# Kernel tuning notes

Hardware: AMD Instinct MI355X
Metric: run time of the kernel (lower is better)

Reference implementation:

```python
import jax, jax.numpy as jnp
import numpy as np

N, T, HID, H = 2, 2048, 1024, 16
D = HID // H


def setup_inputs() -> dict:
    key = jax.random.key(0)
    ks = jax.random.split(key, 11)
    s = 1.0 / np.sqrt(HID)
    return {
        "q": jax.random.normal(ks[0], (N, T, HID), jnp.float32),
        "k": jax.random.normal(ks[1], (N, T, HID), jnp.float32),
        "v": jax.random.normal(ks[2], (N, T, HID), jnp.float32),
        "Wq": jax.random.normal(ks[3], (HID, HID), jnp.float32) * s,
        "bq": jnp.zeros((HID,), jnp.float32),
        "Wk": jax.random.normal(ks[4], (HID, HID), jnp.float32) * s,
        "bk": jnp.zeros((HID,), jnp.float32),
        "Wv": jax.random.normal(ks[5], (HID, HID), jnp.float32) * s,
        "bv": jnp.zeros((HID,), jnp.float32),
        "Wo": jax.random.normal(ks[6], (HID, HID), jnp.float32) * s,
        "bo": jnp.zeros((HID,), jnp.float32),
    }


def reference(q, k, v, Wq, bq, Wk, bk, Wv, bv, Wo, bo):
    n, t, _ = q.shape
    # Linear projections, then the original's quirky head split:
    # .view(N, H, T, D) directly from (N, T, H*D) (no transpose).
    qh = (q @ Wq + bq).reshape(n, H, t, D)
    kh = (k @ Wk + bk).reshape(n, H, t, D)
    vh = (v @ Wv + bv).reshape(n, H, t, D)
    # scores: (N, H, T, T), scaled by sqrt(hidden_size) (not head dim)
    scores = jnp.einsum("nhtd,nhsd->nhts", qh, kh) / jnp.sqrt(jnp.float32(HID))
    # faithful quirk: softmax over dim=1 (the head axis)
    attn = jax.nn.softmax(scores, axis=1)
    # dropout is identity (eval / drop_rate=0)
    out = jnp.einsum("nhts,nhsd->nhtd", attn, vh).reshape(n, t, H * D)
    return out @ Wo + bo
```

## Files before the change

kernel.cpp:

```cpp
#include <hip/hip_runtime.h>

typedef unsigned short u16;
typedef __bf16 bf16x8 __attribute__((ext_vector_type(8)));
typedef float f32x4 __attribute__((ext_vector_type(4)));

#define MFMA16 __builtin_amdgcn_mfma_f32_16x16x32_bf16

constexpr int NB = 2, TS = 2048, HD = 1024, NH = 16, DH = 64;
constexpr float ALPHA = 0.045084220027780106f;

__device__ __forceinline__ u16 f2bf(float f) {
    union { float f; unsigned u; } v; v.f = f;
    unsigned r = v.u + 0x7FFFu + ((v.u >> 16) & 1u);
    return (u16)(r >> 16);
}
__device__ __forceinline__ float bf2f(u16 h) {
    union { unsigned u; float f; } v; v.u = ((unsigned)h) << 16;
    return v.f;
}
__device__ __forceinline__ bf16x8 ldb8(const u16* p) {
    return *reinterpret_cast<const bf16x8*>(p);
}
__device__ __forceinline__ void glds16(const u16* g, u16* l) {
    __builtin_amdgcn_global_load_lds(
        (const __attribute__((address_space(1))) unsigned int*)g,
        (__attribute__((address_space(3))) unsigned int*)l, 16, 0, 0);
}

#if defined(__has_builtin)
#  if __has_builtin(__builtin_amdgcn_cvt_pk_bf16_f32)
#    define HAVE_PKBF16 1
#  endif
#  if __has_builtin(__builtin_amdgcn_exp2f)
#    define HAVE_EXP2 1
#  endif
#endif
#ifndef HAVE_PKBF16
#  define HAVE_PKBF16 0
#endif
#ifndef HAVE_EXP2
#  define HAVE_EXP2 0
#endif
__device__ __forceinline__ unsigned pk2(float a, float b) {
#if HAVE_PKBF16
    typedef __bf16 bf16x2 __attribute__((ext_vector_type(2)));
    bf16x2 r = __builtin_amdgcn_cvt_pk_bf16_f32(a, b);
    return __builtin_bit_cast(unsigned, r);
#else
    return (unsigned)f2bf(a) | ((unsigned)f2bf(b) << 16);
#endif
}
__device__ __forceinline__ float fexp2(float x) {
#if HAVE_EXP2
    return __builtin_amdgcn_exp2f(x);
#else
    return exp2f(x);
#endif
}

__global__ __launch_bounds__(256) void to_bf16(
    const float* __restrict__ a0, const float* __restrict__ a1, const float* __restrict__ a2,
    u16* __restrict__ o0, u16* __restrict__ o1, u16* __restrict__ o2)
{
    const float* s; u16* d;
    if (blockIdx.y == 0)      { s = a0; d = o0; }
    else if (blockIdx.y == 1) { s = a1; d = o1; }
    else                      { s = a2; d = o2; }
    size_t i = ((size_t)blockIdx.x * 256 + threadIdx.x) * 8;
    float4 v0 = *reinterpret_cast<const float4*>(s + i);
    float4 v1 = *reinterpret_cast<const float4*>(s + i + 4);
    uint4 w = { pk2(v0.x, v0.y), pk2(v0.z, v0.w), pk2(v1.x, v1.y), pk2(v1.z, v1.w) };
    *reinterpret_cast<uint4*>(d + i) = w;
}

__global__ __launch_bounds__(256) void wtrans(
    const float* __restrict__ w0, const float* __restrict__ w1,
    const float* __restrict__ w2, const float* __restrict__ w3,
    u16* __restrict__ o0, u16* __restrict__ o1,
    u16* __restrict__ o2, u16* __restrict__ o3)
{
    const float* src; u16* dst; float sc;
    if (blockIdx.z == 0)      { src = w0; dst = o0; sc = ALPHA; }
    else if (blockIdx.z == 1) { src = w1; dst = o1; sc = 1.0f; }
    else if (blockIdx.z == 2) { src = w2; dst = o2; sc = 1.0f; }
    else                      { src = w3; dst = o3; sc = 1.0f; }
    __shared__ __align__(16) u16 tile[64 * 72];
    const int k0 = blockIdx.y * 64, n0 = blockIdx.x * 64;
    const int t = threadIdx.x, r = t >> 2, c0 = (t & 3) << 4;
#pragma unroll
    for (int j = 0; j < 4; ++j) {
        float4 v = *reinterpret_cast<const float4*>(&src[(size_t)(k0 + r) * HD + n0 + c0 + 4 * j]);
        tile[(c0 + 4 * j + 0) * 72 + r] = f2bf(v.x * sc);
        tile[(c0 + 4 * j + 1) * 72 + r] = f2bf(v.y * sc);
        tile[(c0 + 4 * j + 2) * 72 + r] = f2bf(v.z * sc);
        tile[(c0 + 4 * j + 3) * 72 + r] = f2bf(v.w * sc);
    }
    __syncthreads();
#pragma unroll
    for (int j = 0; j < 2; ++j)
        *reinterpret_cast<uint4*>(&dst[(size_t)(n0 + r) * HD + k0 + c0 + 8 * j]) =
            *reinterpret_cast<const uint4*>(&tile[r * 72 + c0 + 8 * j]);
}

__global__ __launch_bounds__(256) void gemm_qkv(
    const u16* __restrict__ A0, const u16* __restrict__ A1, const u16* __restrict__ A2,
    const u16* __restrict__ B0, const u16* __restrict__ B1, const u16* __restrict__ B2,
    const float* __restrict__ c0, const float* __restrict__ c1, const float* __restrict__ c2,
    u16* __restrict__ C0, u16* __restrict__ C1, u16* __restrict__ C2)
{
    const u16 *A, *BT; const float* bias; u16* C; float bsc;
    if (blockIdx.z == 0)      { A = A0; BT = B0; bias = c0; C = C0; bsc = ALPHA; }
    else if (blockIdx.z == 1) { A = A1; BT = B1; bias = c1; C = C1; bsc = 1.0f; }
    else                      { A = A2; BT = B2; bias = c2; C = C2; bsc = 1.0f; }
    constexpr int N = HD, K = HD;
    __shared__ __align__(16) u16 As[128 * 32];
    __shared__ __align__(16) u16 Bs[128 * 32];
    const int m0 = blockIdx.y * 128, n0 = blockIdx.x * 128;
    const int tid = threadIdx.x, wid = tid >> 6, lane = tid & 63;
    const int q = lane >> 4, c = lane & 15;
    const int wm = wid >> 1, wn = wid & 1;
    const int srow = tid >> 2, scol = (tid & 3) << 3;
    const u16* ag0 = A + (size_t)(m0 + srow) * K + scol;
    const u16* ag1 = A + (size_t)(m0 + 64 + srow) * K + scol;
    const u16* bg0 = BT + (size_t)(n0 + srow) * K + scol;
    const u16* bg1 = BT + (size_t)(n0 + 64 + srow) * K + scol;
    f32x4 acc[4][4] = {};
    for (int k0 = 0; k0 < K; k0 += 32) {
        glds16(ag0, &As[tid * 8]);
        glds16(ag1, &As[2048 + tid * 8]);
        glds16(bg0, &Bs[tid * 8]);
        glds16(bg1, &Bs[2048 + tid * 8]);
        ag0 += 32; ag1 += 32; bg0 += 32; bg1 += 32;
        __syncthreads();
        bf16x8 af[4], bf[4];
#pragma unroll
        for (int i = 0; i < 4; ++i)  af[i] = ldb8(&As[(wm * 64 + i * 16 + c) * 32 + q * 8]);
#pragma unroll
        for (int jn = 0; jn < 4; ++jn) bf[jn] = ldb8(&Bs[(wn * 64 + jn * 16 + c) * 32 + q * 8]);
#pragma unroll
        for (int i = 0; i < 4; ++i)
#pragma unroll
            for (int jn = 0; jn < 4; ++jn)
                acc[i][jn] = MFMA16(bf[jn], af[i], acc[i][jn], 0, 0, 0);
        __syncthreads();
    }
#pragma unroll
    for (int i = 0; i < 4; ++i)
#pragma unroll
        for (int jn = 0; jn < 4; ++jn) {
            int row = m0 + wm * 64 + i * 16 + c;
            int col = n0 + wn * 64 + jn * 16 + q * 4;
            float4 bb = *reinterpret_cast<const float4*>(&bias[col]);
            uint2 w = { pk2(acc[i][jn][0] + bb.x * bsc, acc[i][jn][1] + bb.y * bsc),
                        pk2(acc[i][jn][2] + bb.z * bsc, acc[i][jn][3] + bb.w * bsc) };
            *reinterpret_cast<uint2*>(&C[(size_t)row * N + col]) = w;
        }
}

__global__ __launch_bounds__(256) void vtrans(const u16* __restrict__ V, u16* __restrict__ VT)
{
    __shared__ __align__(16) u16 tile[64 * 72];
    const int nh = blockIdx.y, t0 = blockIdx.x * 64;
    const u16* src = V + (size_t)nh * TS * DH;
    u16* dst = VT + (size_t)nh * DH * TS;
    const int t = threadIdx.x, r = t >> 2, c0 = (t & 3) << 4;
    *reinterpret_cast<uint4*>(&tile[r * 72 + c0]) =
        *reinterpret_cast<const uint4*>(&src[(size_t)(t0 + r) * DH + c0]);
    *reinterpret_cast<uint4*>(&tile[r * 72 + c0 + 8]) =
        *reinterpret_cast<const uint4*>(&src[(size_t)(t0 + r) * DH + c0 + 8]);
    __syncthreads();
    const int d = t >> 2, tc = (t & 3) << 4;
    u16 tmp[16];
#pragma unroll
    for (int j = 0; j < 16; ++j) tmp[j] = tile[(tc + j) * 72 + d];
    *reinterpret_cast<uint4*>(&dst[(size_t)d * TS + t0 + tc]) = *reinterpret_cast<const uint4*>(&tmp[0]);
    *reinterpret_cast<uint4*>(&dst[(size_t)d * TS + t0 + tc + 8]) = *reinterpret_cast<const uint4*>(&tmp[8]);
}

__global__ __launch_bounds__(256) void gemm_out(
    const u16* __restrict__ A, const u16* __restrict__ BT,
    const float* __restrict__ bias, float* __restrict__ C,
    int M, int N, int K)
{
    __shared__ __align__(16) u16 As[64 * 32];
    __shared__ __align__(16) u16 Bs[128 * 32];
    const int m0 = blockIdx.y * 64, n0 = blockIdx.x * 128;
    const int tid = threadIdx.x, wid = tid >> 6, lane = tid & 63;
    const int q = lane >> 4, c = lane & 15;
    const int wm = wid >> 1, wn = wid & 1;
    const int arow = tid >> 2, acol = (tid & 3) << 3;
    const u16* ag = A + (size_t)(m0 + arow) * K + acol;
    const u16* bg0 = BT + (size_t)(n0 + arow) * K + acol;
    const u16* bg1 = BT + (size_t)(n0 + 64 + arow) * K + acol;
    f32x4 acc[2][4] = {};
    for (int k0 = 0; k0 < K; k0 += 32) {
        glds16(ag, &As[tid * 8]);
        glds16(bg0, &Bs[tid * 8]);
        glds16(bg1, &Bs[2048 + tid * 8]);
        ag += 32; bg0 += 32; bg1 += 32;
        __syncthreads();
        bf16x8 af[2], bf[4];
#pragma unroll
        for (int jm = 0; jm < 2; ++jm) af[jm] = ldb8(&As[(wm * 32 + jm * 16 + c) * 32 + q * 8]);
#pragma unroll
        for (int jn = 0; jn < 4; ++jn) bf[jn] = ldb8(&Bs[(wn * 64 + jn * 16 + c) * 32 + q * 8]);
#pragma unroll
        for (int jm = 0; jm < 2; ++jm)
#pragma unroll
            for (int jn = 0; jn < 4; ++jn)
                acc[jm][jn] = MFMA16(bf[jn], af[jm], acc[jm][jn], 0, 0, 0);
        __syncthreads();
    }
#pragma unroll
    for (int jm = 0; jm < 2; ++jm)
#pragma unroll
        for (int jn = 0; jn < 4; ++jn) {
            int row = m0 + wm * 32 + jm * 16 + c;
            int col = n0 + wn * 64 + jn * 16 + q * 4;
            float4 bb = *reinterpret_cast<const float4*>(&bias[col]);
            float4 v = { acc[jm][jn][0] + bb.x, acc[jm][jn][1] + bb.y,
                         acc[jm][jn][2] + bb.z, acc[jm][jn][3] + bb.w };
            *reinterpret_cast<float4*>(&C[(size_t)row * N + col]) = v;
        }
}

__global__ __launch_bounds__(256) void z_kernel(
    const u16* __restrict__ Qp, const u16* __restrict__ Kp, u16* __restrict__ Zf)
{
    __shared__ __align__(16) u16 Ks[64 * 64];
    __shared__ __align__(16) u16 Qs[128 * 64];
    const int sb = blockIdx.x, tb = blockIdx.y, n = blockIdx.z;
    const int s0 = sb * 64, t0 = tb * 128;
    const int tid = threadIdx.x, wid = tid >> 6, lane = tid & 63;
    const int q = lane >> 4, c = lane & 15;
    const int krow = tid >> 3, kch = tid & 7;
    const int xsw = (kch ^ (krow & 7)) << 3;
    const u16* kg0 = Kp + (size_t)(n * NH) * TS * DH + (size_t)(s0 + krow) * DH + xsw;
    const u16* qg0 = Qp + (size_t)(n * NH) * TS * DH + (size_t)(t0 + krow) * DH + xsw;
    float zacc[2][4][4] = {};
    for (int h = 0; h < NH; ++h) {
        glds16(kg0, &Ks[tid * 8]);
        glds16(kg0 + (size_t)32 * DH, &Ks[2048 + tid * 8]);
#pragma unroll
        for (int L = 0; L < 4; ++L)
            glds16(qg0 + (size_t)(L * 32) * DH, &Qs[L * 2048 + tid * 8]);
        kg0 += (size_t)TS * DH; qg0 += (size_t)TS * DH;
        __syncthreads();
        bf16x8 qa[2][2], kb[4][2];
#pragma unroll
        for (int jm = 0; jm < 2; ++jm)
#pragma unroll
            for (int kf = 0; kf < 2; ++kf)
                qa[jm][kf] = ldb8(&Qs[(wid * 32 + jm * 16 + c) * 64 + (((kf * 4 + q) ^ (c & 7)) << 3)]);
#pragma unroll
        for (int i = 0; i < 4; ++i)
#pragma unroll
            for (int kf = 0; kf < 2; ++kf)
                kb[i][kf] = ldb8(&Ks[(i * 16 + c) * 64 + (((kf * 4 + q) ^ (c & 7)) << 3)]);
        f32x4 s_[2][4] = {};
#pragma unroll
        for (int kf = 0; kf < 2; ++kf)
#pragma unroll
            for (int jm = 0; jm < 2; ++jm)
#pragma unroll
                for (int i = 0; i < 4; ++i)
                    s_[jm][i] = MFMA16(kb[i][kf], qa[jm][kf], s_[jm][i], 0, 0, 0);
#pragma unroll
        for (int jm = 0; jm < 2; ++jm)
#pragma unroll
            for (int i = 0; i < 4; ++i)
#pragma unroll
                for (int r = 0; r < 4; ++r)
                    zacc[jm][i][r] += fexp2(s_[jm][i][r]);
        __syncthreads();
    }
#pragma unroll
    for (int jm = 0; jm < 2; ++jm) {
        int t = t0 + wid * 32 + jm * 16 + c;
        size_t zb = ((size_t)((n * 32 + sb) * 2048) + t) * 64 + q * 16;
        unsigned w32[8];
#pragma unroll
        for (int i = 0; i < 4; ++i) {
            w32[i * 2 + 0] = pk2(1.0f / zacc[jm][i][0], 1.0f / zacc[jm][i][1]);
            w32[i * 2 + 1] = pk2(1.0f / zacc[jm][i][2], 1.0f / zacc[jm][i][3]);
        }
        *reinterpret_cast<uint4*>(&Zf[zb])     = *reinterpret_cast<const uint4*>(&w32[0]);
        *reinterpret_cast<uint4*>(&Zf[zb + 8]) = *reinterpret_cast<const uint4*>(&w32[4]);
    }
}

__global__ __launch_bounds__(256) void attn_kernel(
    const u16* __restrict__ Qp, const u16* __restrict__ Kp, const u16* __restrict__ VT,
    const u16* __restrict__ Zf, u16* __restrict__ o2)
{
    __shared__ __align__(16) u16 Ks[64 * 64];
    __shared__ __align__(16) u16 Vs[64 * 64];
    __shared__ __align__(16) u16 Ps[64 * 72];
    const int tb = blockIdx.x, h = blockIdx.y, n = blockIdx.z;
    const int t0 = tb * 64;
    const int tid = threadIdx.x, wid = tid >> 6, lane = tid & 63;
    const int q = lane >> 4, c = lane & 15;
    const int krow = tid >> 3, kch = tid & 7;
    const int xsw = (kch ^ (krow & 7)) << 3;
    const size_t base = (size_t)(n * NH + h) * TS * DH;
    const u16* Qh = Qp + base;
    const int tme = t0 + wid * 16 + c;
    bf16x8 qa[2];
#pragma unroll
    for (int kf = 0; kf < 2; ++kf)
        qa[kf] = ldb8(&Qh[(size_t)tme * DH + kf * 32 + q * 8]);
    const u16* kg0 = Kp + base + (size_t)krow * DH + xsw;
    const u16* kg1 = kg0 + (size_t)32 * DH;
    const u16* vg0 = VT + base + (size_t)krow * TS + xsw;
    const u16* vg1 = vg0 + (size_t)32 * TS;
    const u16* zg  = Zf + ((size_t)(n * 32) * 2048 + tme) * 64 + q * 16;
    f32x4 oacc[4] = {};
    for (int sb = 0; sb < 32; ++sb) {
        glds16(kg0, &Ks[tid * 8]);
        glds16(kg1, &Ks[2048 + tid * 8]);
        glds16(vg0, &Vs[tid * 8]);
        glds16(vg1, &Vs[2048 + tid * 8]);
        u16 zl[16];
        *reinterpret_cast<uint4*>(&zl[0]) = *reinterpret_cast<const uint4*>(zg);
        *reinterpret_cast<uint4*>(&zl[8]) = *reinterpret_cast<const uint4*>(zg + 8);
        kg0 += 64 * DH; kg1 += 64 * DH; vg0 += 64; vg1 += 64; zg += (size_t)2048 * 64;
        __syncthreads();
        bf16x8 kb[4][2];
#pragma unroll
        for (int i = 0; i < 4; ++i)
#pragma unroll
            for (int kf = 0; kf < 2; ++kf)
                kb[i][kf] = ldb8(&Ks[(i * 16 + c) * 64 + (((kf * 4 + q) ^ (c & 7)) << 3)]);
        f32x4 s_[4] = {};
#pragma unroll
        for (int kf = 0; kf < 2; ++kf)
#pragma unroll
            for (int i = 0; i < 4; ++i)
                s_[i] = MFMA16(kb[i][kf], qa[kf], s_[i], 0, 0, 0);
#pragma unroll
        for (int i = 0; i < 4; ++i) {
            float p0 = fexp2(s_[i][0]) * bf2f(zl[i * 4 + 0]);
            float p1 = fexp2(s_[i][1]) * bf2f(zl[i * 4 + 1]);
            float p2 = fexp2(s_[i][2]) * bf2f(zl[i * 4 + 2]);
            float p3 = fexp2(s_[i][3]) * bf2f(zl[i * 4 + 3]);
            uint2 w = { pk2(p0, p1), pk2(p2, p3) };
            *reinterpret_cast<uint2*>(&Ps[(wid * 16 + c) * 72 + i * 16 + q * 4]) = w;
        }
        bf16x8 pa[2], vb[4][2];
#pragma unroll
        for (int kf = 0; kf < 2; ++kf)
            pa[kf] = ldb8(&Ps[(wid * 16 + c) * 72 + kf * 32 + q * 8]);
#pragma unroll
        for (int dn = 0; dn < 4; ++dn)
#pragma unroll
            for (int kf = 0; kf < 2; ++kf)
                vb[dn][kf] = ldb8(&Vs[(dn * 16 + c) * 64 + (((kf * 4 + q) ^ (c & 7)) << 3)]);
#pragma unroll
        for (int kf = 0; kf < 2; ++kf)
#pragma unroll
            for (int dn = 0; dn < 4; ++dn)
                oacc[dn] = MFMA16(vb[dn][kf], pa[kf], oacc[dn], 0, 0, 0);
        __syncthreads();
    }
#pragma unroll
    for (int dn = 0; dn < 4; ++dn) {
        uint2 w = { pk2(oacc[dn][0], oacc[dn][1]), pk2(oacc[dn][2], oacc[dn][3]) };
        *reinterpret_cast<uint2*>(&o2[base + (size_t)tme * DH + dn * 16 + q * 4]) = w;
    }
}

extern "C" void kernel_launch(void* const* d_in, const int* in_sizes, int n_in,
                              void* d_out, int out_size, void* d_ws, size_t ws_size,
                              hipStream_t stream)
{
    const float* q  = (const float*)d_in[0];
    const float* k  = (const float*)d_in[1];
    const float* v  = (const float*)d_in[2];
    const float* Wq = (const float*)d_in[3];
    const float* bq = (const float*)d_in[4];
    const float* Wk = (const float*)d_in[5];
    const float* bk = (const float*)d_in[6];
    const float* Wv = (const float*)d_in[7];
    const float* bv = (const float*)d_in[8];
    const float* Wo = (const float*)d_in[9];
    const float* bo = (const float*)d_in[10];
    float* out = (float*)d_out;

    u16* ws  = (u16*)d_ws;
    u16* wqT = ws + 0 * 1048576;
    u16* wkT = ws + 1 * 1048576;
    u16* wvT = ws + 2 * 1048576;
    u16* woT = ws + 3 * 1048576;
    u16* S1  = ws + 4194304;
    u16* S2  = S1 + 4194304;
    u16* S3  = S2 + 4194304;
    u16* S4  = S3 + 4194304;
    u16* S5  = S4 + 4194304;
    u16* S6  = S5 + 4194304;
    u16 *qb = S1, *kb = S2, *vb = S3;
    u16 *Qp = S4, *Kp = S5, *Vp = S6;
    u16 *VTb = S1, *Zf = S2, *o2 = S6;

    to_bf16<<<dim3(2048, 3), 256, 0, stream>>>(q, k, v, qb, kb, vb);
    wtrans<<<dim3(16, 16, 4), 256, 0, stream>>>(Wq, Wk, Wv, Wo, wqT, wkT, wvT, woT);
    gemm_qkv<<<dim3(8, 32, 3), 256, 0, stream>>>(qb, kb, vb, wqT, wkT, wvT,
                                                 bq, bk, bv, Qp, Kp, Vp);
    vtrans<<<dim3(32, 32), 256, 0, stream>>>(Vp, VTb);
    z_kernel<<<dim3(32, 16, 2), 256, 0, stream>>>(Qp, Kp, Zf);
    attn_kernel<<<dim3(32, 16, 2), 256, 0, stream>>>(Qp, Kp, VTb, Zf, o2);
    gemm_out<<<dim3(8, 64), 256, 0, stream>>>(o2, woT, bo, out, NB * TS, HD, HD);
}
```

Measured before the change: 295.4 us.

## Merge prep kernels, widen GEMM K-tiles, double-buffer attention and Z loads

Merges the input bf16 conversion and weight transpose into one launch. Both GEMMs now use a 64-wide K step with XOR-swizzled shared memory, which halves the number of barriers per tile. The attention and Z kernels double-buffer their K/V shared tiles so the next block loads while the current one computes. The Z kernel also reads Q fragments straight from global memory instead of staging them in LDS. The cost is more LDS use per block, which may lower occupancy, and Q reads in the Z kernel are no longer coalesced through shared memory.

New measurement: 325.4 us. 10.2% more time.

```diff
diff --git a/kernel.cpp b/kernel.cpp
--- a/kernel.cpp
+++ b/kernel.cpp
@@ -58,34 +58,36 @@
 #endif
 }
 
-__global__ __launch_bounds__(256) void to_bf16(
+__global__ __launch_bounds__(256) void prep(
     const float* __restrict__ a0, const float* __restrict__ a1, const float* __restrict__ a2,
-    u16* __restrict__ o0, u16* __restrict__ o1, u16* __restrict__ o2)
-{
-    const float* s; u16* d;
-    if (blockIdx.y == 0)      { s = a0; d = o0; }
-    else if (blockIdx.y == 1) { s = a1; d = o1; }
-    else                      { s = a2; d = o2; }
-    size_t i = ((size_t)blockIdx.x * 256 + threadIdx.x) * 8;
-    float4 v0 = *reinterpret_cast<const float4*>(s + i);
-    float4 v1 = *reinterpret_cast<const float4*>(s + i + 4);
-    uint4 w = { pk2(v0.x, v0.y), pk2(v0.z, v0.w), pk2(v1.x, v1.y), pk2(v1.z, v1.w) };
-    *reinterpret_cast<uint4*>(d + i) = w;
-}
-
-__global__ __launch_bounds__(256) void wtrans(
+    u16* __restrict__ o0, u16* __restrict__ o1, u16* __restrict__ o2,
     const float* __restrict__ w0, const float* __restrict__ w1,
     const float* __restrict__ w2, const float* __restrict__ w3,
-    u16* __restrict__ o0, u16* __restrict__ o1,
-    u16* __restrict__ o2, u16* __restrict__ o3)
-{
-    const float* src; u16* dst; float sc;
-    if (blockIdx.z == 0)      { src = w0; dst = o0; sc = ALPHA; }
-    else if (blockIdx.z == 1) { src = w1; dst = o1; sc = 1.0f; }
-    else if (blockIdx.z == 2) { src = w2; dst = o2; sc = 1.0f; }
-    else                      { src = w3; dst = o3; sc = 1.0f; }
+    u16* __restrict__ wo0, u16* __restrict__ wo1,
+    u16* __restrict__ wo2, u16* __restrict__ wo3)
+{
     __shared__ __align__(16) u16 tile[64 * 72];
-    const int k0 = blockIdx.y * 64, n0 = blockIdx.x * 64;
+    if (blockIdx.z < 3) {
+        const float* s; u16* d;
+        if (blockIdx.z == 0)      { s = a0; d = o0; }
+        else if (blockIdx.z == 1) { s = a1; d = o1; }
+        else                      { s = a2; d = o2; }
+        size_t i = ((size_t)blockIdx.x * 256 + threadIdx.x) * 8;
+        float4 v0 = *reinterpret_cast<const float4*>(s + i);
+        float4 v1 = *reinterpret_cast<const float4*>(s + i + 4);
+        uint4 w = { pk2(v0.x, v0.y), pk2(v0.z, v0.w), pk2(v1.x, v1.y), pk2(v1.z, v1.w) };
+        *reinterpret_cast<uint4*>(d + i) = w;
+        return;
+    }
+    if (blockIdx.x >= 1024) return;
+    const int wi = blockIdx.x >> 8, ti = blockIdx.x & 255;
+    const int ky = ti >> 4, nx = ti & 15;
+    const float* src; u16* dst; float sc = 1.0f;
+    if (wi == 0)      { src = w0; dst = wo0; sc = ALPHA; }
+    else if (wi == 1) { src = w1; dst = wo1; }
+    else if (wi == 2) { src = w2; dst = wo2; }
+    else              { src = w3; dst = wo3; }
+    const int k0 = ky * 64, n0 = nx * 64;
     const int t = threadIdx.x, r = t >> 2, c0 = (t & 3) << 4;
 #pragma unroll
     for (int j = 0; j < 4; ++j) {
@@ -113,35 +115,40 @@
     else if (blockIdx.z == 1) { A = A1; BT = B1; bias = c1; C = C1; bsc = 1.0f; }
     else                      { A = A2; BT = B2; bias = c2; C = C2; bsc = 1.0f; }
     constexpr int N = HD, K = HD;
-    __shared__ __align__(16) u16 As[128 * 32];
-    __shared__ __align__(16) u16 Bs[128 * 32];
+    __shared__ __align__(16) u16 As[128 * 64];
+    __shared__ __align__(16) u16 Bs[128 * 64];
     const int m0 = blockIdx.y * 128, n0 = blockIdx.x * 128;
     const int tid = threadIdx.x, wid = tid >> 6, lane = tid & 63;
     const int q = lane >> 4, c = lane & 15;
     const int wm = wid >> 1, wn = wid & 1;
-    const int srow = tid >> 2, scol = (tid & 3) << 3;
-    const u16* ag0 = A + (size_t)(m0 + srow) * K + scol;
-    const u16* ag1 = A + (size_t)(m0 + 64 + srow) * K + scol;
-    const u16* bg0 = BT + (size_t)(n0 + srow) * K + scol;
-    const u16* bg1 = BT + (size_t)(n0 + 64 + srow) * K + scol;
+    const int r = tid >> 3, ch = tid & 7;
+    const int xc = (ch ^ (r & 7)) << 3;
+    const u16* ag = A + (size_t)(m0 + r) * K + xc;
+    const u16* bg = BT + (size_t)(n0 + r) * K + xc;
     f32x4 acc[4][4] = {};
-    for (int k0 = 0; k0 < K; k0 += 32) {
-        glds16(ag0, &As[tid * 8]);
-        glds16(ag1, &As[2048 + tid * 8]);
-        glds16(bg0, &Bs[tid * 8]);
-        glds16(bg1, &Bs[2048 + tid * 8]);
-        ag0 += 32; ag1 += 32; bg0 += 32; bg1 += 32;
-        __syncthreads();
-        bf16x8 af[4], bf[4];
-#pragma unroll
-        for (int i = 0; i < 4; ++i)  af[i] = ldb8(&As[(wm * 64 + i * 16 + c) * 32 + q * 8]);
-#pragma unroll
-        for (int jn = 0; jn < 4; ++jn) bf[jn] = ldb8(&Bs[(wn * 64 + jn * 16 + c) * 32 + q * 8]);
+    for (int k0 = 0; k0 < K; k0 += 64) {
+#pragma unroll
+        for (int L = 0; L < 4; ++L) {
+            glds16(ag + (size_t)(32 * L) * K, &As[L * 2048 + tid * 8]);
+            glds16(bg + (size_t)(32 * L) * K, &Bs[L * 2048 + tid * 8]);
+        }
+        ag += 64; bg += 64;
+        __syncthreads();
+        bf16x8 af[4][2], bf[4][2];
 #pragma unroll
         for (int i = 0; i < 4; ++i)
 #pragma unroll
-            for (int jn = 0; jn < 4; ++jn)
-                acc[i][jn] = MFMA16(bf[jn], af[i], acc[i][jn], 0, 0, 0);
+            for (int kk = 0; kk < 2; ++kk) {
+                af[i][kk] = ldb8(&As[(wm * 64 + i * 16 + c) * 64 + (((kk * 4 + q) ^ (c & 7)) << 3)]);
+                bf[i][kk] = ldb8(&Bs[(wn * 64 + i * 16 + c) * 64 + (((kk * 4 + q) ^ (c & 7)) << 3)]);
+            }
+#pragma unroll
+        for (int kk = 0; kk < 2; ++kk)
+#pragma unroll
+            for (int i = 0; i < 4; ++i)
+#pragma unroll
+                for (int jn = 0; jn < 4; ++jn)
+                    acc[i][jn] = MFMA16(bf[jn][kk], af[i][kk], acc[i][jn], 0, 0, 0);
         __syncthreads();
     }
 #pragma unroll
@@ -182,33 +189,43 @@
     const float* __restrict__ bias, float* __restrict__ C,
     int M, int N, int K)
 {
-    __shared__ __align__(16) u16 As[64 * 32];
-    __shared__ __align__(16) u16 Bs[128 * 32];
+    __shared__ __align__(16) u16 As[64 * 64];
+    __shared__ __align__(16) u16 Bs[128 * 64];
     const int m0 = blockIdx.y * 64, n0 = blockIdx.x * 128;
     const int tid = threadIdx.x, wid = tid >> 6, lane = tid & 63;
     const int q = lane >> 4, c = lane & 15;
     const int wm = wid >> 1, wn = wid & 1;
-    const int arow = tid >> 2, acol = (tid & 3) << 3;
-    const u16* ag = A + (size_t)(m0 + arow) * K + acol;
-    const u16* bg0 = BT + (size_t)(n0 + arow) * K + acol;
-    const u16* bg1 = BT + (size_t)(n0 + 64 + arow) * K + acol;
+    const int r = tid >> 3, ch = tid & 7;
+    const int xc = (ch ^ (r & 7)) << 3;
+    const u16* ag = A + (size_t)(m0 + r) * K + xc;
+    const u16* bg = BT + (size_t)(n0 + r) * K + xc;
     f32x4 acc[2][4] = {};
-    for (int k0 = 0; k0 < K; k0 += 32) {
+    for (int k0 = 0; k0 < K; k0 += 64) {
         glds16(ag, &As[tid * 8]);
-        glds16(bg0, &Bs[tid * 8]);
-        glds16(bg1, &Bs[2048 + tid * 8]);
-        ag += 32; bg0 += 32; bg1 += 32;
-        __syncthreads();
-        bf16x8 af[2], bf[4];
-#pragma unroll
-        for (int jm = 0; jm < 2; ++jm) af[jm] = ldb8(&As[(wm * 32 + jm * 16 + c) * 32 + q * 8]);
-#pragma unroll
-        for (int jn = 0; jn < 4; ++jn) bf[jn] = ldb8(&Bs[(wn * 64 + jn * 16 + c) * 32 + q * 8]);
+        glds16(ag + (size_t)32 * K, &As[2048 + tid * 8]);
+#pragma unroll
+        for (int L = 0; L < 4; ++L)
+            glds16(bg + (size_t)(32 * L) * K, &Bs[L * 2048 + tid * 8]);
+        ag += 64; bg += 64;
+        __syncthreads();
+        bf16x8 af[2][2], bf[4][2];
 #pragma unroll
         for (int jm = 0; jm < 2; ++jm)
 #pragma unroll
-            for (int jn = 0; jn < 4; ++jn)
-                acc[jm][jn] = MFMA16(bf[jn], af[jm], acc[jm][jn], 0, 0, 0);
+            for (int kk = 0; kk < 2; ++kk)
+                af[jm][kk] = ldb8(&As[(wm * 32 + jm * 16 + c) * 64 + (((kk * 4 + q) ^ (c & 7)) << 3)]);
+#pragma unroll
+        for (int jn = 0; jn < 4; ++jn)
+#pragma unroll
+            for (int kk = 0; kk < 2; ++kk)
+                bf[jn][kk] = ldb8(&Bs[(wn * 64 + jn * 16 + c) * 64 + (((kk * 4 + q) ^ (c & 7)) << 3)]);
+#pragma unroll
+        for (int kk = 0; kk < 2; ++kk)
+#pragma unroll
+            for (int jm = 0; jm < 2; ++jm)
+#pragma unroll
+                for (int jn = 0; jn < 4; ++jn)
+                    acc[jm][jn] = MFMA16(bf[jn][kk], af[jm][kk], acc[jm][jn], 0, 0, 0);
         __syncthreads();
     }
 #pragma unroll
@@ -227,36 +244,39 @@
 __global__ __launch_bounds__(256) void z_kernel(
     const u16* __restrict__ Qp, const u16* __restrict__ Kp, u16* __restrict__ Zf)
 {
-    __shared__ __align__(16) u16 Ks[64 * 64];
-    __shared__ __align__(16) u16 Qs[128 * 64];
+    __shared__ __align__(16) u16 Ks[2 * 64 * 64];
     const int sb = blockIdx.x, tb = blockIdx.y, n = blockIdx.z;
     const int s0 = sb * 64, t0 = tb * 128;
     const int tid = threadIdx.x, wid = tid >> 6, lane = tid & 63;
     const int q = lane >> 4, c = lane & 15;
     const int krow = tid >> 3, kch = tid & 7;
     const int xsw = (kch ^ (krow & 7)) << 3;
-    const u16* kg0 = Kp + (size_t)(n * NH) * TS * DH + (size_t)(s0 + krow) * DH + xsw;
-    const u16* qg0 = Qp + (size_t)(n * NH) * TS * DH + (size_t)(t0 + krow) * DH + xsw;
+    const u16* kg = Kp + (size_t)(n * NH) * TS * DH + (size_t)(s0 + krow) * DH + xsw;
+    const u16* Qh = Qp + (size_t)(n * NH) * TS * DH;
+    glds16(kg, &Ks[tid * 8]);
+    glds16(kg + (size_t)32 * DH, &Ks[2048 + tid * 8]);
+    kg += (size_t)TS * DH;
     float zacc[2][4][4] = {};
     for (int h = 0; h < NH; ++h) {
-        glds16(kg0, &Ks[tid * 8]);
-        glds16(kg0 + (size_t)32 * DH, &Ks[2048 + tid * 8]);
-#pragma unroll
-        for (int L = 0; L < 4; ++L)
-            glds16(qg0 + (size_t)(L * 32) * DH, &Qs[L * 2048 + tid * 8]);
-        kg0 += (size_t)TS * DH; qg0 += (size_t)TS * DH;
-        __syncthreads();
+        u16* Kc = &Ks[(h & 1) * 4096];
+        __syncthreads();
+        if (h + 1 < NH) {
+            u16* Kn = &Ks[((h + 1) & 1) * 4096];
+            glds16(kg, &Kn[tid * 8]);
+            glds16(kg + (size_t)32 * DH, &Kn[2048 + tid * 8]);
+            kg += (size_t)TS * DH;
+        }
         bf16x8 qa[2][2], kb[4][2];
 #pragma unroll
         for (int jm = 0; jm < 2; ++jm)
 #pragma unroll
             for (int kf = 0; kf < 2; ++kf)
-                qa[jm][kf] = ldb8(&Qs[(wid * 32 + jm * 16 + c) * 64 + (((kf * 4 + q) ^ (c & 7)) << 3)]);
+                qa[jm][kf] = ldb8(&Qh[(size_t)(t0 + wid * 32 + jm * 16 + c) * DH + kf * 32 + q * 8]);
 #pragma unroll
         for (int i = 0; i < 4; ++i)
 #pragma unroll
             for (int kf = 0; kf < 2; ++kf)
-                kb[i][kf] = ldb8(&Ks[(i * 16 + c) * 64 + (((kf * 4 + q) ^ (c & 7)) << 3)]);
+                kb[i][kf] = ldb8(&Kc[(i * 16 + c) * 64 + (((kf * 4 + q) ^ (c & 7)) << 3)]);
         f32x4 s_[2][4] = {};
 #pragma unroll
         for (int kf = 0; kf < 2; ++kf)
@@ -272,7 +292,7 @@
 #pragma unroll
                 for (int r = 0; r < 4; ++r)
                     zacc[jm][i][r] += fexp2(s_[jm][i][r]);
-        __syncthreads();
+        Qh += (size_t)TS * DH;
     }
 #pragma unroll
     for (int jm = 0; jm < 2; ++jm) {
@@ -293,8 +313,8 @@
     const u16* __restrict__ Qp, const u16* __restrict__ Kp, const u16* __restrict__ VT,
     const u16* __restrict__ Zf, u16* __restrict__ o2)
 {
-    __shared__ __align__(16) u16 Ks[64 * 64];
-    __shared__ __align__(16) u16 Vs[64 * 64];
+    __shared__ __align__(16) u16 Ks[2 * 64 * 64];
+    __shared__ __align__(16) u16 Vs[2 * 64 * 64];
     __shared__ __align__(16) u16 Ps[64 * 72];
     const int tb = blockIdx.x, h = blockIdx.y, n = blockIdx.z;
     const int t0 = tb * 64;
@@ -303,34 +323,43 @@
     const int krow = tid >> 3, kch = tid & 7;
     const int xsw = (kch ^ (krow & 7)) << 3;
     const size_t base = (size_t)(n * NH + h) * TS * DH;
-    const u16* Qh = Qp + base;
     const int tme = t0 + wid * 16 + c;
     bf16x8 qa[2];
 #pragma unroll
     for (int kf = 0; kf < 2; ++kf)
-        qa[kf] = ldb8(&Qh[(size_t)tme * DH + kf * 32 + q * 8]);
-    const u16* kg0 = Kp + base + (size_t)krow * DH + xsw;
-    const u16* kg1 = kg0 + (size_t)32 * DH;
-    const u16* vg0 = VT + base + (size_t)krow * TS + xsw;
-    const u16* vg1 = vg0 + (size_t)32 * TS;
-    const u16* zg  = Zf + ((size_t)(n * 32) * 2048 + tme) * 64 + q * 16;
+        qa[kf] = ldb8(&Qp[base + (size_t)tme * DH + kf * 32 + q * 8]);
+    const u16* kg = Kp + base + (size_t)krow * DH + xsw;
+    const u16* vg = VT + base + (size_t)krow * TS + xsw;
+    const u16* zg = Zf + ((size_t)(n * 32) * 2048 + tme) * 64 + q * 16;
+    glds16(kg, &Ks[tid * 8]);
+    glds16(kg + (size_t)32 * DH, &Ks[2048 + tid * 8]);
+    glds16(vg, &Vs[tid * 8]);
+    glds16(vg + (size_t)32 * TS, &Vs[2048 + tid * 8]);
+    kg += 64 * DH; vg += 64;
     f32x4 oacc[4] = {};
     for (int sb = 0; sb < 32; ++sb) {
-        glds16(kg0, &Ks[tid * 8]);
-        glds16(kg1, &Ks[2048 + tid * 8]);
-        glds16(vg0, &Vs[tid * 8]);
-        glds16(vg1, &Vs[2048 + tid * 8]);
+        u16* Kc = &Ks[(sb & 1) * 4096];
+        u16* Vc = &Vs[(sb & 1) * 4096];
+        __syncthreads();
+        if (sb + 1 < 32) {
+            u16* Kn = &Ks[((sb + 1) & 1) * 4096];
+            u16* Vn = &Vs[((sb + 1) & 1) * 4096];
+            glds16(kg, &Kn[tid * 8]);
+            glds16(kg + (size_t)32 * DH, &Kn[2048 + tid * 8]);
+            glds16(vg, &Vn[tid * 8]);
+            glds16(vg + (size_t)32 * TS, &Vn[2048 + tid * 8]);
+            kg += 64 * DH; vg += 64;
+        }
         u16 zl[16];
         *reinterpret_cast<uint4*>(&zl[0]) = *reinterpret_cast<const uint4*>(zg);
         *reinterpret_cast<uint4*>(&zl[8]) = *reinterpret_cast<const uint4*>(zg + 8);
-        kg0 += 64 * DH; kg1 += 64 * DH; vg0 += 64; vg1 += 64; zg += (size_t)2048 * 64;
-        __syncthreads();
+        zg += (size_t)2048 * 64;
         bf16x8 kb[4][2];
 #pragma unroll
         for (int i = 0; i < 4; ++i)
 #pragma unroll
             for (int kf = 0; kf < 2; ++kf)
-                kb[i][kf] = ldb8(&Ks[(i * 16 + c) * 64 + (((kf * 4 + q) ^ (c & 7)) << 3)]);
+                kb[i][kf] = ldb8(&Kc[(i * 16 + c) * 64 + (((kf * 4 + q) ^ (c & 7)) << 3)]);
         f32x4 s_[4] = {};
 #pragma unroll
         for (int kf = 0; kf < 2; ++kf)
@@ -354,13 +383,12 @@
         for (int dn = 0; dn < 4; ++dn)
 #pragma unroll
             for (int kf = 0; kf < 2; ++kf)
-                vb[dn][kf] = ldb8(&Vs[(dn * 16 + c) * 64 + (((kf * 4 + q) ^ (c & 7)) << 3)]);
+                vb[dn][kf] = ldb8(&Vc[(dn * 16 + c) * 64 + (((kf * 4 + q) ^ (c & 7)) << 3)]);
 #pragma unroll
         for (int kf = 0; kf < 2; ++kf)
 #pragma unroll
             for (int dn = 0; dn < 4; ++dn)
                 oacc[dn] = MFMA16(vb[dn][kf], pa[kf], oacc[dn], 0, 0, 0);
-        __syncthreads();
     }
 #pragma unroll
     for (int dn = 0; dn < 4; ++dn) {
@@ -401,8 +429,8 @@
     u16 *Qp = S4, *Kp = S5, *Vp = S6;
     u16 *VTb = S1, *Zf = S2, *o2 = S6;
 
-    to_bf16<<<dim3(2048, 3), 256, 0, stream>>>(q, k, v, qb, kb, vb);
-    wtrans<<<dim3(16, 16, 4), 256, 0, stream>>>(Wq, Wk, Wv, Wo, wqT, wkT, wvT, woT);
+    prep<<<dim3(2048, 1, 4), 256, 0, stream>>>(q, k, v, qb, kb, vb,
+                                               Wq, Wk, Wv, Wo, wqT, wkT, wvT, woT);
     gemm_qkv<<<dim3(8, 32, 3), 256, 0, stream>>>(qb, kb, vb, wqT, wkT, wvT,
                                                  bq, bk, bv, Qp, Kp, Vp);
     vtrans<<<dim3(32, 32), 256, 0, stream>>>(Vp, VTb);
```
